# Kernel tuning notes

Measured on AMD Instinct MI355X. Metric: run time of the kernel, lower is better.

Reference implementation:

```python
import jax, jax.numpy as jnp
import numpy as np

PRED_LEN = 24
F, I, H = 64, 128, 512  # features_size, input_size, hidden_size
B, S = 1024, 168        # batch, seq_len


def setup_inputs() -> dict:
    key = jax.random.key(0)
    ks = jax.random.split(key, 14)
    s = 0.05
    return {
        "x": jax.random.normal(ks[0], (B, S, F), dtype=jnp.float32),
        "W_enc": jax.random.normal(ks[1], (I, F), dtype=jnp.float32) * s,
        "b_enc": jax.random.normal(ks[2], (I,), dtype=jnp.float32) * s,
        "Wih0": jax.random.normal(ks[3], (4 * H, I), dtype=jnp.float32) * s,
        "Whh0": jax.random.normal(ks[4], (4 * H, H), dtype=jnp.float32) * s,
        "bih0": jax.random.normal(ks[5], (4 * H,), dtype=jnp.float32) * s,
        "bhh0": jax.random.normal(ks[6], (4 * H,), dtype=jnp.float32) * s,
        "Wih1": jax.random.normal(ks[7], (4 * H, H), dtype=jnp.float32) * s,
        "Whh1": jax.random.normal(ks[8], (4 * H, H), dtype=jnp.float32) * s,
        "bih1": jax.random.normal(ks[9], (4 * H,), dtype=jnp.float32) * s,
        "bhh1": jax.random.normal(ks[10], (4 * H,), dtype=jnp.float32) * s,
        "W_dec": jax.random.normal(ks[11], (F, H), dtype=jnp.float32) * s,
        "b_dec": jax.random.normal(ks[12], (F,), dtype=jnp.float32) * s,
    }


def _lstm_cell(xt, h, c, Wih, Whh, bih, bhh):
    # PyTorch gate order: i, f, g, o
    gates = xt @ Wih.T + h @ Whh.T + (bih + bhh)
    i, f, g, o = jnp.split(gates, 4, axis=-1)
    c = jax.nn.sigmoid(f) * c + jax.nn.sigmoid(i) * jnp.tanh(g)
    h = jax.nn.sigmoid(o) * jnp.tanh(c)
    return h, c


def reference(x, W_enc, b_enc, Wih0, Whh0, bih0, bhh0,
              Wih1, Whh1, bih1, bhh1, W_dec, b_dec):
    batch = x.shape[0]
    h0 = jnp.zeros((batch, H), x.dtype)
    init = (h0, h0, h0, h0)  # (h_l0, c_l0, h_l1, c_l1)

    def step(carry, xt):
        hl0, cl0, hl1, cl1 = carry
        enc = xt @ W_enc.T + b_enc
        hl0, cl0 = _lstm_cell(enc, hl0, cl0, Wih0, Whh0, bih0, bhh0)
        hl1, cl1 = _lstm_cell(hl0, hl1, cl1, Wih1, Whh1, bih1, bhh1)
        out = hl1 @ W_dec.T + b_dec
        return (hl0, cl0, hl1, cl1), out

    # teacher-forced pass over the observed sequence; keep only last output
    carry, outs = jax.lax.scan(step, init, jnp.transpose(x, (1, 0, 2)))
    last = outs[-1]  # [B, F], prediction for step seq_len (idx = seq_len-1)

    def ar_step(state, _):
        carry, prev = state
        carry, out = step(carry, prev)
        return (carry, out), out

    _, ar_outs = jax.lax.scan(ar_step, (carry, last), None, length=PRED_LEN - 1)
    outputs = jnp.concatenate([last[None], ar_outs], axis=0)  # [pred_len, B, F]
    return jnp.transpose(outputs, (1, 0, 2))  # [B, pred_len, F]
```

## Files before the change

### kernel.cpp

```cpp
#include <hip/hip_runtime.h>

#define B_   1024
#define S_   168
#define F_   64
#define I_   128
#define H_   512
#define G4   2048
#define PRED 24

typedef unsigned short u16;
typedef unsigned int   u32;
typedef __attribute__((ext_vector_type(8))) __bf16 bf16x8;
typedef __attribute__((ext_vector_type(4))) float  f32x4;
typedef __attribute__((ext_vector_type(4))) int    i32x4;

__device__ __forceinline__ u16 f2bf(float f) {
  u32 u = __float_as_uint(f);
  u += 0x7fff + ((u >> 16) & 1);
  return (u16)(u >> 16);
}
__device__ __forceinline__ float bf2f(u16 h) {
  return __uint_as_float(((u32)h) << 16);
}
__device__ __forceinline__ float sigm(float x) {
  x = fminf(fmaxf(x, -30.f), 30.f);
  return 1.f / (1.f + __expf(-x));
}
__device__ __forceinline__ float tanh_(float x) {
  x = fminf(fmaxf(x, -15.f), 15.f);
  float e = __expf(2.f * x);
  return (e - 1.f) / (e + 1.f);
}


__global__ void k_split(const float* __restrict__ src, u16* __restrict__ hi,
                        u16* __restrict__ lo, int n) {
  for (int i = blockIdx.x * 256 + threadIdx.x; i < n; i += gridDim.x * 256) {
    float a = src[i];
    u16 h = f2bf(a);
    hi[i] = h;
    lo[i] = f2bf(a - bf2f(h));
  }
}

__global__ void k_w0c(const float* __restrict__ Wih0, const float* __restrict__ Wenc,
                      float* __restrict__ W0c) {
  int id = blockIdx.x * 256 + threadIdx.x;
  int j = id >> 6, f = id & 63;
  float s = 0.f;
  for (int i = 0; i < 128; ++i) s += Wih0[j * 128 + i] * Wenc[i * 64 + f];
  W0c[id] = s;
}

__global__ void k_w0cd(const float* __restrict__ W0c, const float* __restrict__ Wdec,
                       float* __restrict__ W0cd) {
  int id = blockIdx.x * 256 + threadIdx.x;
  int j = id >> 9, m = id & 511;
  float s = 0.f;
  for (int f = 0; f < 64; ++f) s += W0c[j * 64 + f] * Wdec[f * 512 + m];
  W0cd[id] = s;
}

__global__ void k_biases(const float* __restrict__ Wih0, const float* __restrict__ benc,
                         const float* __restrict__ bih0, const float* __restrict__ bhh0,
                         const float* __restrict__ bih1, const float* __restrict__ bhh1,
                         float* __restrict__ b0c, float* __restrict__ b1c) {
  int j = blockIdx.x * 256 + threadIdx.x;
  float s = 0.f;
  for (int i = 0; i < 128; ++i) s += Wih0[j * 128 + i] * benc[i];
  b0c[j] = s + bih0[j] + bhh0[j];
  b1c[j] = bih1[j] + bhh1[j];
}

__global__ void k_b0ar(const float* __restrict__ W0c, const float* __restrict__ bdec,
                       const float* __restrict__ b0c, float* __restrict__ b0ar) {
  int j = blockIdx.x * 256 + threadIdx.x;
  float s = 0.f;
  for (int f = 0; f < 64; ++f) s += W0c[j * 64 + f] * bdec[f];
  b0ar[j] = b0c[j] + s;
}

__global__ void k_pack(const float* __restrict__ W, int K, u16* __restrict__ dst) {
  int id = blockIdx.x * 256 + threadIdx.x;
  int lane = id & 63, fi = id >> 6;
  int NK = K >> 5;
  int kt = fi % NK, jg = fi / NK;
  int g = jg & 3, jt = jg >> 2;
  int j = jt * 16 + (lane & 15);
  int kb = kt * 32 + (lane >> 4) * 8;
  const float* src = W + (size_t)(g * 512 + j) * K + kb;
  u16 hi[8] __attribute__((aligned(16)));
  u16 lo[8] __attribute__((aligned(16)));
#pragma unroll
  for (int e = 0; e < 8; ++e) {
    float v = src[e];
    u16 h = f2bf(v);
    hi[e] = h;
    lo[e] = f2bf(v - bf2f(h));
  }
  u16* d = dst + (size_t)fi * 1024 + lane * 8;
  *(i32x4*)d = *(const i32x4*)hi;
  *(i32x4*)(d + 512) = *(const i32x4*)lo;
}


struct CellArgs {
  const u16* A1hi; const u16* A1lo; int strideA1; int K1;
  const u16* W1p;
  const u16* A2hi; const u16* A2lo;
  const u16* W2p;
  const float* bias;
  float* c;
  u16* hhi; u16* hlo;
};

struct DecArgs {
  const u16* hhi; const u16* hlo;
  const float* Wdec; const float* bdec;
  float* out;
};

__device__ __forceinline__ void cell_body(const CellArgs& P, u16* smem_,
                                          int t, int jblk, int mblk) {
  const u16* __restrict__ A1hi = P.A1hi;
  const u16* __restrict__ A1lo = P.A1lo;
  const int strideA1 = P.strideA1;
  const int K1 = P.K1;
  const u16* __restrict__ W1p = P.W1p;
  const u16* __restrict__ A2hi = P.A2hi;
  const u16* __restrict__ A2lo = P.A2lo;
  const u16* __restrict__ W2p = P.W2p;
  const float* __restrict__ bias = P.bias;
  float* __restrict__ c = P.c;
  u16* __restrict__ hhi = P.hhi;
  u16* __restrict__ hlo = P.hlo;

  const int mbase = mblk * 64;
  const int lane = t & 63, wv = t >> 6;
  const int kk = wv >> 1, jh = wv & 1;
  const int lr = lane & 15, qk = lane >> 4;
  const int jtg = jblk * 2 + jh;
  const int nc1 = (K1 == 64) ? 1 : 4;
  const int NC  = nc1 + 4;
  const int NK1 = K1 >> 5;

  f32x4 acc[4][4];
#pragma unroll
  for (int mi = 0; mi < 4; ++mi)
#pragma unroll
    for (int g = 0; g < 4; ++g) acc[mi][g] = (f32x4){0.f, 0.f, 0.f, 0.f};

  auto prm = [&](int cc, const u16*& Ah, const u16*& Al, int& st, int& kb, int& Kc,
                 const u16*& Wp, int& NK) {
    if (cc < nc1) { Ah = A1hi; Al = A1lo; st = strideA1; kb = cc * 128;
                    Kc = (K1 == 64) ? 64 : 128; Wp = W1p; NK = NK1; }
    else { int i = cc - nc1; Ah = A2hi; Al = A2lo; st = 512; kb = i * 128;
           Kc = 128; Wp = W2p; NK = 16; }
  };
  auto nsof = [&](int cc) { return (cc < nc1 && K1 == 64) ? 2 : 4; };

  auto stageLoad = [&](int cc, i32x4* rr) {
    const u16 *Ah, *Al, *Wp_; int st, kb, Kc, NK;
    prm(cc, Ah, Al, st, kb, Kc, Wp_, NK);
    const int ppr = Kc >> 3;
    const int npc = (Kc == 128) ? 4 : 2;
#pragma unroll 4
    for (int p = 0; p < npc; ++p) {
      int li   = p * 512 + t;
      int part = li >= 64 * ppr;
      int liw  = li - part * 64 * ppr;
      int rown = (ppr == 16) ? (liw >> 4) : (liw >> 3);
      int kp   = liw & (ppr - 1);
      const u16* src = (part ? Al : Ah) + (size_t)(mbase + rown) * st + kb + kp * 8;
      rr[p] = *(const i32x4*)src;
    }
  };
  auto stageWrite = [&](int cc, const i32x4* rr, int buf) {
    const int Kc  = (cc < nc1 && K1 == 64) ? 64 : 128;
    const int ppr = Kc >> 3;
    const int npc = (Kc == 128) ? 4 : 2;
    u16* sb = smem_ + buf * 16384;
#pragma unroll 4
    for (int p = 0; p < npc; ++p) {
      int li   = p * 512 + t;
      int part = li >= 64 * ppr;
      int liw  = li - part * 64 * ppr;
      int rown = (ppr == 16) ? (liw >> 4) : (liw >> 3);
      int kp   = liw & (ppr - 1);
      *(i32x4*)&sb[(((part * 64 + rown) * ppr) + (kp ^ (rown & (ppr - 1)))) * 8] = rr[p];
    }
  };
  auto loadW = [&](const u16* Wp_, int NK, int kt, i32x4* wh, i32x4* wl) {
#pragma unroll
    for (int g = 0; g < 4; ++g) {
      const u16* p = Wp_ + (size_t)((jtg * 4 + g) * NK + kt) * 1024 + lane * 8;
      wh[g] = *(const i32x4*)p;
      wl[g] = *(const i32x4*)(p + 512);
    }
  };
  auto mstep = [&](int buf, int ppr, const i32x4* wh, const i32x4* wl) {
    const u16* sb = smem_ + buf * 16384;
    bf16x8 ah[4], al[4];
#pragma unroll
    for (int mi = 0; mi < 4; ++mi) {
      int rowA = mi * 16 + lr;
      int pl   = (kk * 4 + qk) ^ (rowA & (ppr - 1));
      ah[mi] = *(const bf16x8*)&sb[(rowA * ppr + pl) * 8];
      al[mi] = *(const bf16x8*)&sb[((64 + rowA) * ppr + pl) * 8];
    }
#pragma unroll
    for (int g = 0; g < 4; ++g) {
      bf16x8 bh = __builtin_bit_cast(bf16x8, wh[g]);
      bf16x8 bl = __builtin_bit_cast(bf16x8, wl[g]);
#pragma unroll
      for (int mi = 0; mi < 4; ++mi) {
        acc[mi][g] = __builtin_amdgcn_mfma_f32_16x16x32_bf16(ah[mi], bh, acc[mi][g], 0, 0, 0);
        acc[mi][g] = __builtin_amdgcn_mfma_f32_16x16x32_bf16(al[mi], bh, acc[mi][g], 0, 0, 0);
        acc[mi][g] = __builtin_amdgcn_mfma_f32_16x16x32_bf16(ah[mi], bl, acc[mi][g], 0, 0, 0);
      }
    }
  };

  i32x4 sreg[4];
  i32x4 whA[4], wlA[4], whB[4], wlB[4];

  stageLoad(0, sreg);
  stageWrite(0, sreg, 0);
  {
    const u16 *Ah, *Al, *Wp_; int st, kb, Kc, NK;
    prm(0, Ah, Al, st, kb, Kc, Wp_, NK);
    if (kk < nsof(0)) loadW(Wp_, NK, (kb >> 5) + kk, whA, wlA);
  }
  __syncthreads();

  for (int cc = 0; cc < NC; ++cc) {
    const int buf  = cc & 1;
    const bool more = (cc + 1 < NC);
    if (more) {
      stageLoad(cc + 1, sreg);
      const u16 *Ah, *Al, *Wp_; int st, kb, Kc, NK;
      prm(cc + 1, Ah, Al, st, kb, Kc, Wp_, NK);
      if (kk < nsof(cc + 1)) loadW(Wp_, NK, (kb >> 5) + kk, whB, wlB);
    }
    {
      const u16 *Ah, *Al, *Wp_; int st, kb, Kc, NK;
      prm(cc, Ah, Al, st, kb, Kc, Wp_, NK);
      if (kk < nsof(cc)) mstep(buf, Kc >> 3, whA, wlA);
    }
    if (more) stageWrite(cc + 1, sreg, buf ^ 1);
    __syncthreads();
    if (more) {
#pragma unroll
      for (int g = 0; g < 4; ++g) { whA[g] = whB[g]; wlA[g] = wlB[g]; }
    }
  }

  float* red = (float*)smem_;
#pragma unroll
  for (int mi = 0; mi < 4; ++mi) {
    if (mi != kk) {
      int slot = kk - (kk > mi ? 1 : 0);
      float* base = red + (size_t)(((jh * 4 + mi) * 3 + slot) * 1024) + lane * 4;
#pragma unroll
      for (int g = 0; g < 4; ++g) *(f32x4*)(base + g * 256) = acc[mi][g];
    }
  }
  __syncthreads();

  f32x4 r[4];
#pragma unroll
  for (int g = 0; g < 4; ++g) r[g] = acc[0][g];
  if (kk == 1) {
#pragma unroll
    for (int g = 0; g < 4; ++g) r[g] = acc[1][g];
  } else if (kk == 2) {
#pragma unroll
    for (int g = 0; g < 4; ++g) r[g] = acc[2][g];
  } else if (kk == 3) {
#pragma unroll
    for (int g = 0; g < 4; ++g) r[g] = acc[3][g];
  }
#pragma unroll
  for (int s = 0; s < 3; ++s) {
    float* base = red + (size_t)(((jh * 4 + kk) * 3 + s) * 1024) + lane * 4;
#pragma unroll
    for (int g = 0; g < 4; ++g) r[g] += *(const f32x4*)(base + g * 256);
  }

  const int   j   = jblk * 32 + jh * 16 + lr;
  const float bi  = bias[j];
  const float bff = bias[512 + j];
  const float bg  = bias[1024 + j];
  const float bo  = bias[1536 + j];
#pragma unroll
  for (int rr = 0; rr < 4; ++rr) {
    int b   = mbase + kk * 16 + qk * 4 + rr;
    int idx = b * 512 + j;
    float iv = sigm(r[0][rr] + bi);
    float fv = sigm(r[1][rr] + bff);
    float gv = tanh_(r[2][rr] + bg);
    float ov = sigm(r[3][rr] + bo);
    float cn = fv * c[idx] + iv * gv;
    c[idx] = cn;
    float hn = ov * tanh_(cn);
    u16 hh = f2bf(hn);
    hhi[idx] = hh;
    hlo[idx] = f2bf(hn - bf2f(hh));
  }
}

__device__ __forceinline__ void dec_body(const DecArgs& D, float* smemf,
                                         int t, int bx, int by) {
  if (by >= 8) return;
  float (*sH)[65] = (float (*)[65])smemf;
  const int bbase = bx * 64;
  const int mbase = by * 64;
  {
    int b  = bbase + (t >> 3);
    int m0 = (t & 7) * 8;
    i32x4 hv = *(const i32x4*)&D.hhi[(size_t)b * 512 + mbase + m0];
    i32x4 lv = *(const i32x4*)&D.hlo[(size_t)b * 512 + mbase + m0];
    const u16* hp = (const u16*)&hv;
    const u16* lp = (const u16*)&lv;
#pragma unroll
    for (int e = 0; e < 8; ++e)
      sH[t >> 3][m0 + e] = bf2f(hp[e]) + bf2f(lp[e]);
  }
  __syncthreads();
  const int bl = t & 63;
  const int wv = t >> 6;
  float acc[8];
#pragma unroll
  for (int u = 0; u < 8; ++u) acc[u] = 0.f;
  for (int m = 0; m < 64; ++m) {
    float hv = sH[bl][m];
#pragma unroll
    for (int u = 0; u < 8; ++u)
      acc[u] += hv * D.Wdec[(size_t)(u * 8 + wv) * 512 + mbase + m];
  }
#pragma unroll
  for (int u = 0; u < 8; ++u) {
    int f = u * 8 + wv;
    float v = acc[u];
    if (by == 0) v += D.bdec[f];
    atomicAdd(&D.out[(size_t)(bbase + bl) * (PRED * F_) + f], v);
  }
}


__global__ __launch_bounds__(512, 2) void lstm3(CellArgs a) {
  __shared__ __align__(16) u16 smem_[49152];
  cell_body(a, smem_, threadIdx.x, blockIdx.x, blockIdx.y);
}

__global__ __launch_bounds__(512, 2) void lstm3_dual(CellArgs a0, CellArgs a1) {
  __shared__ __align__(16) u16 smem_[49152];
  if (blockIdx.z == 0) cell_body(a0, smem_, threadIdx.x, blockIdx.x, blockIdx.y);
  else                 cell_body(a1, smem_, threadIdx.x, blockIdx.x, blockIdx.y);
}

__global__ __launch_bounds__(512, 2) void lstm3_cell_dec(CellArgs a, DecArgs d) {
  __shared__ __align__(16) u16 smem_[49152];
  if (blockIdx.z == 0) cell_body(a, smem_, threadIdx.x, blockIdx.x, blockIdx.y);
  else                 dec_body(d, (float*)smem_, threadIdx.x, blockIdx.x, blockIdx.y);
}

__global__ __launch_bounds__(512) void k_decoder2(DecArgs d) {
  __shared__ __align__(16) float sm[64 * 65];
  dec_body(d, sm, threadIdx.x, blockIdx.x, blockIdx.y);
}


extern "C" void kernel_launch(void* const* d_in, const int* in_sizes, int n_in,
                              void* d_out, int out_size, void* d_ws, size_t ws_size,
                              hipStream_t stream) {
  const float* x    = (const float*)d_in[0];
  const float* Wenc = (const float*)d_in[1];
  const float* benc = (const float*)d_in[2];
  const float* Wih0 = (const float*)d_in[3];
  const float* Whh0 = (const float*)d_in[4];
  const float* bih0 = (const float*)d_in[5];
  const float* bhh0 = (const float*)d_in[6];
  const float* Wih1 = (const float*)d_in[7];
  const float* Whh1 = (const float*)d_in[8];
  const float* bih1 = (const float*)d_in[9];
  const float* bhh1 = (const float*)d_in[10];
  const float* Wdec = (const float*)d_in[11];
  const float* bdec = (const float*)d_in[12];
  float* out = (float*)d_out;

  char* p = (char*)d_ws;
  auto carve = [&](size_t bytes) { char* r = p; p += (bytes + 255) & ~(size_t)255; return r; };
  const size_t NX = (size_t)B_ * S_ * F_;
  const size_t NH = (size_t)B_ * H_;
  const size_t WP512 = (size_t)G4 * 512 * 2;
  u16* Xhi    = (u16*)carve(NX * 2);
  u16* Xlo    = (u16*)carve(NX * 2);
  float* W0c  = (float*)carve((size_t)G4 * 64 * 4);
  float* W0cd = (float*)carve((size_t)G4 * 512 * 4);
  u16* W0cp   = (u16*)carve((size_t)G4 * 64 * 2 * 2);
  u16* W0cdp  = (u16*)carve(WP512 * 2);
  u16* Whh0p  = (u16*)carve(WP512 * 2);
  u16* Wih1p  = (u16*)carve(WP512 * 2);
  u16* Whh1p  = (u16*)carve(WP512 * 2);
  float* b0c  = (float*)carve(G4 * 4);
  float* b0ar = (float*)carve(G4 * 4);
  float* b1c  = (float*)carve(G4 * 4);
  u16* h0hi[2] = {(u16*)carve(NH * 2), (u16*)carve(NH * 2)};
  u16* h0lo[2] = {(u16*)carve(NH * 2), (u16*)carve(NH * 2)};
  u16* h1hi[2] = {(u16*)carve(NH * 2), (u16*)carve(NH * 2)};
  u16* h1lo[2] = {(u16*)carve(NH * 2), (u16*)carve(NH * 2)};
  float* c0 = (float*)carve(NH * 4);
  float* c1 = (float*)carve(NH * 4);
  (void)ws_size; (void)n_in; (void)in_sizes;

  hipMemsetAsync(d_out, 0, (size_t)out_size * 4, stream);
  hipMemsetAsync(h0hi[0], 0, NH * 2, stream);
  hipMemsetAsync(h0lo[0], 0, NH * 2, stream);
  hipMemsetAsync(h1hi[0], 0, NH * 2, stream);
  hipMemsetAsync(h1lo[0], 0, NH * 2, stream);
  hipMemsetAsync(c0, 0, NH * 4, stream);
  hipMemsetAsync(c1, 0, NH * 4, stream);

  k_split<<<4096, 256, 0, stream>>>(x, Xhi, Xlo, (int)NX);
  k_w0c<<<512, 256, 0, stream>>>(Wih0, Wenc, W0c);
  k_w0cd<<<4096, 256, 0, stream>>>(W0c, Wdec, W0cd);
  k_biases<<<8, 256, 0, stream>>>(Wih0, benc, bih0, bhh0, bih1, bhh1, b0c, b1c);
  k_b0ar<<<8, 256, 0, stream>>>(W0c, bdec, b0c, b0ar);
  k_pack<<<32 * 16, 256, 0, stream>>>(Whh0, 512, Whh0p);
  k_pack<<<32 * 16, 256, 0, stream>>>(Wih1, 512, Wih1p);
  k_pack<<<32 * 16, 256, 0, stream>>>(Whh1, 512, Whh1p);
  k_pack<<<32 * 16, 256, 0, stream>>>(W0cd, 512, W0cdp);
  k_pack<<<32 * 2, 256, 0, stream>>>(W0c, 64, W0cp);

  dim3 grid(16, 16);
  dim3 grid2(16, 16, 2);

  {
    CellArgs l0 = {Xhi, Xlo, S_ * F_, 64, W0cp,
                   h0hi[0], h0lo[0], Whh0p, b0c, c0, h0hi[1], h0lo[1]};
    lstm3<<<grid, 512, 0, stream>>>(l0);
  }
  for (int s = 0; s < S_ - 1; ++s) {
    int pp = s & 1, np = 1 - pp;
    CellArgs l1 = {h0hi[np], h0lo[np], 512, 512, Wih1p,
                   h1hi[pp], h1lo[pp], Whh1p, b1c, c1, h1hi[np], h1lo[np]};
    CellArgs l0 = {Xhi + (size_t)(s + 1) * F_, Xlo + (size_t)(s + 1) * F_, S_ * F_, 64, W0cp,
                   h0hi[np], h0lo[np], Whh0p, b0c, c0, h0hi[pp], h0lo[pp]};
    lstm3_dual<<<grid2, 512, 0, stream>>>(l1, l0);
  }
  {
    CellArgs l1 = {h0hi[0], h0lo[0], 512, 512, Wih1p,
                   h1hi[1], h1lo[1], Whh1p, b1c, c1, h1hi[0], h1lo[0]};
    lstm3<<<grid, 512, 0, stream>>>(l1);
  }

  for (int s = S_ - 1; s < S_ + PRED - 1; ++s) {
    int pp = s & 1, np = 1 - pp;
    DecArgs d = {h1hi[np], h1lo[np], Wdec, bdec, out + (size_t)(s - (S_ - 1)) * F_};
    if (s + 1 < S_ + PRED - 1) {
      CellArgs l0 = {h1hi[np], h1lo[np], 512, 512, W0cdp,
                     h0hi[np], h0lo[np], Whh0p, b0ar, c0, h0hi[pp], h0lo[pp]};
      lstm3_cell_dec<<<grid2, 512, 0, stream>>>(l0, d);
      CellArgs l1 = {h0hi[pp], h0lo[pp], 512, 512, Wih1p,
                     h1hi[np], h1lo[np], Whh1p, b1c, c1, h1hi[pp], h1lo[pp]};
      lstm3<<<grid, 512, 0, stream>>>(l1);
    } else {
      k_decoder2<<<dim3(16, 8), 512, 0, stream>>>(d);
    }
  }
}
```

Baseline: 7.975 ms.

## Replace per-step kernel launches with a persistent cooperative kernel using grid sync

Replaces about 190 per-timestep kernel launches with one cooperative persistent kernel of 256 blocks that loops over all encoder and autoregressive steps and separates dependent phases with grid.sync(). Layer 1 and layer 0 cells now run one after the other inside each block instead of in parallel across a doubled grid, so each step uses half as many blocks. The goal is to remove launch overhead and inter-kernel gaps. The trade-off is grid-wide barrier cost and the loss of the 2x block parallelism within each step.

```diff
diff --git a/kernel.cpp b/kernel.cpp
--- a/kernel.cpp
+++ b/kernel.cpp
@@ -1,4 +1,7 @@
 #include <hip/hip_runtime.h>
+#include <hip/hip_cooperative_groups.h>
+
+namespace cg = cooperative_groups;
 
 #define B_   1024
 #define S_   168
@@ -348,26 +351,67 @@
 }
 
 
-__global__ __launch_bounds__(512, 2) void lstm3(CellArgs a) {
+struct PersistArgs {
+  const u16* Xhi; const u16* Xlo;
+  const u16 *W0cp, *W0cdp, *Whh0p, *Wih1p, *Whh1p;
+  const float *b0c, *b0ar, *b1c;
+  float *c0, *c1;
+  u16 *h0hi0, *h0hi1, *h0lo0, *h0lo1;
+  u16 *h1hi0, *h1hi1, *h1lo0, *h1lo1;
+  const float *Wdec, *bdec;
+  float* out;
+};
+
+__global__ __launch_bounds__(512, 2) void lstm_persist(PersistArgs A) {
   __shared__ __align__(16) u16 smem_[49152];
-  cell_body(a, smem_, threadIdx.x, blockIdx.x, blockIdx.y);
-}
-
-__global__ __launch_bounds__(512, 2) void lstm3_dual(CellArgs a0, CellArgs a1) {
-  __shared__ __align__(16) u16 smem_[49152];
-  if (blockIdx.z == 0) cell_body(a0, smem_, threadIdx.x, blockIdx.x, blockIdx.y);
-  else                 cell_body(a1, smem_, threadIdx.x, blockIdx.x, blockIdx.y);
-}
-
-__global__ __launch_bounds__(512, 2) void lstm3_cell_dec(CellArgs a, DecArgs d) {
-  __shared__ __align__(16) u16 smem_[49152];
-  if (blockIdx.z == 0) cell_body(a, smem_, threadIdx.x, blockIdx.x, blockIdx.y);
-  else                 dec_body(d, (float*)smem_, threadIdx.x, blockIdx.x, blockIdx.y);
-}
-
-__global__ __launch_bounds__(512) void k_decoder2(DecArgs d) {
-  __shared__ __align__(16) float sm[64 * 65];
-  dec_body(d, sm, threadIdx.x, blockIdx.x, blockIdx.y);
+  cg::grid_group grid = cg::this_grid();
+  const int t    = threadIdx.x;
+  const int bid  = blockIdx.x;
+  const int jblk = bid & 15, mblk = bid >> 4;
+
+  for (int s = -1; s <= S_ - 1; ++s) {
+    const int pp = s & 1;
+    u16* h0hiP = pp ? A.h0hi1 : A.h0hi0;  u16* h0loP = pp ? A.h0lo1 : A.h0lo0;
+    u16* h0hiN = pp ? A.h0hi0 : A.h0hi1;  u16* h0loN = pp ? A.h0lo0 : A.h0lo1;
+    u16* h1hiP = pp ? A.h1hi1 : A.h1hi0;  u16* h1loP = pp ? A.h1lo1 : A.h1lo0;
+    u16* h1hiN = pp ? A.h1hi0 : A.h1hi1;  u16* h1loN = pp ? A.h1lo0 : A.h1lo1;
+    if (s >= 0) {
+      CellArgs l1 = {h0hiN, h0loN, 512, 512, A.Wih1p,
+                     h1hiP, h1loP, A.Whh1p, A.b1c, A.c1, h1hiN, h1loN};
+      cell_body(l1, smem_, t, jblk, mblk);
+      __syncthreads();
+    }
+    if (s + 1 < S_) {
+      CellArgs l0 = {A.Xhi + (size_t)(s + 1) * F_, A.Xlo + (size_t)(s + 1) * F_,
+                     S_ * F_, 64, A.W0cp,
+                     h0hiN, h0loN, A.Whh0p, A.b0c, A.c0, h0hiP, h0loP};
+      cell_body(l0, smem_, t, jblk, mblk);
+    }
+    grid.sync();
+  }
+
+  for (int s = S_ - 1; s < S_ + PRED - 1; ++s) {
+    const int pp = s & 1;
+    u16* h0hiP = pp ? A.h0hi1 : A.h0hi0;  u16* h0loP = pp ? A.h0lo1 : A.h0lo0;
+    u16* h0hiN = pp ? A.h0hi0 : A.h0hi1;  u16* h0loN = pp ? A.h0lo0 : A.h0lo1;
+    u16* h1hiP = pp ? A.h1hi1 : A.h1hi0;  u16* h1loP = pp ? A.h1lo1 : A.h1lo0;
+    u16* h1hiN = pp ? A.h1hi0 : A.h1hi1;  u16* h1loN = pp ? A.h1lo0 : A.h1lo1;
+    DecArgs d = {h1hiN, h1loN, A.Wdec, A.bdec, A.out + (size_t)(s - (S_ - 1)) * F_};
+    if (s + 1 < S_ + PRED - 1) {
+      CellArgs l0 = {h1hiN, h1loN, 512, 512, A.W0cdp,
+                     h0hiN, h0loN, A.Whh0p, A.b0ar, A.c0, h0hiP, h0loP};
+      cell_body(l0, smem_, t, jblk, mblk);
+      __syncthreads();
+      if (bid < 128) dec_body(d, (float*)smem_, t, bid & 15, bid >> 4);
+      grid.sync();
+      CellArgs l1 = {h0hiP, h0loP, 512, 512, A.Wih1p,
+                     h1hiN, h1loN, A.Whh1p, A.b1c, A.c1, h1hiP, h1loP};
+      cell_body(l1, smem_, t, jblk, mblk);
+      grid.sync();
+    } else {
+      if (bid < 128) dec_body(d, (float*)smem_, t, bid & 15, bid >> 4);
+    }
+  }
 }
 
 
@@ -433,40 +477,19 @@
   k_pack<<<32 * 16, 256, 0, stream>>>(W0cd, 512, W0cdp);
   k_pack<<<32 * 2, 256, 0, stream>>>(W0c, 64, W0cp);
 
-  dim3 grid(16, 16);
-  dim3 grid2(16, 16, 2);
-
-  {
-    CellArgs l0 = {Xhi, Xlo, S_ * F_, 64, W0cp,
-                   h0hi[0], h0lo[0], Whh0p, b0c, c0, h0hi[1], h0lo[1]};
-    lstm3<<<grid, 512, 0, stream>>>(l0);
-  }
-  for (int s = 0; s < S_ - 1; ++s) {
-    int pp = s & 1, np = 1 - pp;
-    CellArgs l1 = {h0hi[np], h0lo[np], 512, 512, Wih1p,
-                   h1hi[pp], h1lo[pp], Whh1p, b1c, c1, h1hi[np], h1lo[np]};
-    CellArgs l0 = {Xhi + (size_t)(s + 1) * F_, Xlo + (size_t)(s + 1) * F_, S_ * F_, 64, W0cp,
-                   h0hi[np], h0lo[np], Whh0p, b0c, c0, h0hi[pp], h0lo[pp]};
-    lstm3_dual<<<grid2, 512, 0, stream>>>(l1, l0);
-  }
-  {
-    CellArgs l1 = {h0hi[0], h0lo[0], 512, 512, Wih1p,
-                   h1hi[1], h1lo[1], Whh1p, b1c, c1, h1hi[0], h1lo[0]};
-    lstm3<<<grid, 512, 0, stream>>>(l1);
-  }
-
-  for (int s = S_ - 1; s < S_ + PRED - 1; ++s) {
-    int pp = s & 1, np = 1 - pp;
-    DecArgs d = {h1hi[np], h1lo[np], Wdec, bdec, out + (size_t)(s - (S_ - 1)) * F_};
-    if (s + 1 < S_ + PRED - 1) {
-      CellArgs l0 = {h1hi[np], h1lo[np], 512, 512, W0cdp,
-                     h0hi[np], h0lo[np], Whh0p, b0ar, c0, h0hi[pp], h0lo[pp]};
-      lstm3_cell_dec<<<grid2, 512, 0, stream>>>(l0, d);
-      CellArgs l1 = {h0hi[pp], h0lo[pp], 512, 512, Wih1p,
-                     h1hi[np], h1lo[np], Whh1p, b1c, c1, h1hi[pp], h1lo[pp]};
-      lstm3<<<grid, 512, 0, stream>>>(l1);
-    } else {
-      k_decoder2<<<dim3(16, 8), 512, 0, stream>>>(d);
-    }
-  }
-}
+  PersistArgs pa;
+  pa.Xhi = Xhi; pa.Xlo = Xlo;
+  pa.W0cp = W0cp; pa.W0cdp = W0cdp; pa.Whh0p = Whh0p;
+  pa.Wih1p = Wih1p; pa.Whh1p = Whh1p;
+  pa.b0c = b0c; pa.b0ar = b0ar; pa.b1c = b1c;
+  pa.c0 = c0; pa.c1 = c1;
+  pa.h0hi0 = h0hi[0]; pa.h0hi1 = h0hi[1];
+  pa.h0lo0 = h0lo[0]; pa.h0lo1 = h0lo[1];
+  pa.h1hi0 = h1hi[0]; pa.h1hi1 = h1hi[1];
+  pa.h1lo0 = h1lo[0]; pa.h1lo1 = h1lo[1];
+  pa.Wdec = Wdec; pa.bdec = bdec; pa.out = out;
+
+  void* kargs[] = { (void*)&pa };
+  hipLaunchCooperativeKernel((const void*)lstm_persist, dim3(256), dim3(512),
+                             kargs, 0, stream);
+}
```

New measurement: 16.24 ms. 104% more time.

## Split LSTM cell GEMM across waves by M rows instead of K, drop reduction

Applied to the files above, without the earlier changes.

Each wave now owns one 16-row M slice over the full K range, where before each wave owned a K slice across all 64 rows. This removes the cross-wave LDS reduction and its extra barrier, and shrinks the accumulators from 16 to 4 vectors, so registers and shared memory drop enough for launch bounds of 4 blocks per SM instead of 2. The trade-off is that weight fragments are no longer prefetched a chunk ahead; they are loaded inside the inner k loop, and every wave now reads all the weights, which raises weight traffic per block.

```diff
diff --git a/kernel.cpp b/kernel.cpp
--- a/kernel.cpp
+++ b/kernel.cpp
@@ -137,18 +137,16 @@
 
   const int mbase = mblk * 64;
   const int lane = t & 63, wv = t >> 6;
-  const int kk = wv >> 1, jh = wv & 1;
+  const int mi = wv >> 1, jh = wv & 1;
   const int lr = lane & 15, qk = lane >> 4;
   const int jtg = jblk * 2 + jh;
   const int nc1 = (K1 == 64) ? 1 : 4;
   const int NC  = nc1 + 4;
   const int NK1 = K1 >> 5;
 
-  f32x4 acc[4][4];
-#pragma unroll
-  for (int mi = 0; mi < 4; ++mi)
-#pragma unroll
-    for (int g = 0; g < 4; ++g) acc[mi][g] = (f32x4){0.f, 0.f, 0.f, 0.f};
+  f32x4 acc[4];
+#pragma unroll
+  for (int g = 0; g < 4; ++g) acc[g] = (f32x4){0.f, 0.f, 0.f, 0.f};
 
   auto prm = [&](int cc, const u16*& Ah, const u16*& Al, int& st, int& kb, int& Kc,
                  const u16*& Wp, int& NK) {
@@ -157,7 +155,6 @@
     else { int i = cc - nc1; Ah = A2hi; Al = A2lo; st = 512; kb = i * 128;
            Kc = 128; Wp = W2p; NK = 16; }
   };
-  auto nsof = [&](int cc) { return (cc < nc1 && K1 == 64) ? 2 : 4; };
 
   auto stageLoad = [&](int cc, i32x4* rr) {
     const u16 *Ah, *Al, *Wp_; int st, kb, Kc, NK;
@@ -198,93 +195,46 @@
       wl[g] = *(const i32x4*)(p + 512);
     }
   };
-  auto mstep = [&](int buf, int ppr, const i32x4* wh, const i32x4* wl) {
+  auto mstep = [&](int buf, int ppr, const u16* Wp_, int NK, int kb5) {
     const u16* sb = smem_ + buf * 16384;
-    bf16x8 ah[4], al[4];
-#pragma unroll
-    for (int mi = 0; mi < 4; ++mi) {
-      int rowA = mi * 16 + lr;
-      int pl   = (kk * 4 + qk) ^ (rowA & (ppr - 1));
-      ah[mi] = *(const bf16x8*)&sb[(rowA * ppr + pl) * 8];
-      al[mi] = *(const bf16x8*)&sb[((64 + rowA) * ppr + pl) * 8];
-    }
-#pragma unroll
-    for (int g = 0; g < 4; ++g) {
-      bf16x8 bh = __builtin_bit_cast(bf16x8, wh[g]);
-      bf16x8 bl = __builtin_bit_cast(bf16x8, wl[g]);
-#pragma unroll
-      for (int mi = 0; mi < 4; ++mi) {
-        acc[mi][g] = __builtin_amdgcn_mfma_f32_16x16x32_bf16(ah[mi], bh, acc[mi][g], 0, 0, 0);
-        acc[mi][g] = __builtin_amdgcn_mfma_f32_16x16x32_bf16(al[mi], bh, acc[mi][g], 0, 0, 0);
-        acc[mi][g] = __builtin_amdgcn_mfma_f32_16x16x32_bf16(ah[mi], bl, acc[mi][g], 0, 0, 0);
+    const int nkt  = ppr >> 2;
+    const int rowA = mi * 16 + lr;
+    const int rmask = rowA & (ppr - 1);
+#pragma unroll 4
+    for (int kt = 0; kt < nkt; ++kt) {
+      i32x4 wh[4], wl[4];
+      loadW(Wp_, NK, kb5 + kt, wh, wl);
+      int pl = (kt * 4 + qk) ^ rmask;
+      bf16x8 ah = *(const bf16x8*)&sb[(rowA * ppr + pl) * 8];
+      bf16x8 al = *(const bf16x8*)&sb[((64 + rowA) * ppr + pl) * 8];
+#pragma unroll
+      for (int g = 0; g < 4; ++g) {
+        bf16x8 bh = __builtin_bit_cast(bf16x8, wh[g]);
+        bf16x8 bl = __builtin_bit_cast(bf16x8, wl[g]);
+        acc[g] = __builtin_amdgcn_mfma_f32_16x16x32_bf16(ah, bh, acc[g], 0, 0, 0);
+        acc[g] = __builtin_amdgcn_mfma_f32_16x16x32_bf16(al, bh, acc[g], 0, 0, 0);
+        acc[g] = __builtin_amdgcn_mfma_f32_16x16x32_bf16(ah, bl, acc[g], 0, 0, 0);
       }
     }
   };
 
   i32x4 sreg[4];
-  i32x4 whA[4], wlA[4], whB[4], wlB[4];
 
   stageLoad(0, sreg);
   stageWrite(0, sreg, 0);
-  {
-    const u16 *Ah, *Al, *Wp_; int st, kb, Kc, NK;
-    prm(0, Ah, Al, st, kb, Kc, Wp_, NK);
-    if (kk < nsof(0)) loadW(Wp_, NK, (kb >> 5) + kk, whA, wlA);
-  }
   __syncthreads();
 
   for (int cc = 0; cc < NC; ++cc) {
     const int buf  = cc & 1;
     const bool more = (cc + 1 < NC);
-    if (more) {
-      stageLoad(cc + 1, sreg);
-      const u16 *Ah, *Al, *Wp_; int st, kb, Kc, NK;
-      prm(cc + 1, Ah, Al, st, kb, Kc, Wp_, NK);
-      if (kk < nsof(cc + 1)) loadW(Wp_, NK, (kb >> 5) + kk, whB, wlB);
-    }
+    if (more) stageLoad(cc + 1, sreg);
     {
       const u16 *Ah, *Al, *Wp_; int st, kb, Kc, NK;
       prm(cc, Ah, Al, st, kb, Kc, Wp_, NK);
-      if (kk < nsof(cc)) mstep(buf, Kc >> 3, whA, wlA);
+      mstep(buf, Kc >> 3, Wp_, NK, kb >> 5);
     }
     if (more) stageWrite(cc + 1, sreg, buf ^ 1);
     __syncthreads();
-    if (more) {
-#pragma unroll
-      for (int g = 0; g < 4; ++g) { whA[g] = whB[g]; wlA[g] = wlB[g]; }
-    }
-  }
-
-  float* red = (float*)smem_;
-#pragma unroll
-  for (int mi = 0; mi < 4; ++mi) {
-    if (mi != kk) {
-      int slot = kk - (kk > mi ? 1 : 0);
-      float* base = red + (size_t)(((jh * 4 + mi) * 3 + slot) * 1024) + lane * 4;
-#pragma unroll
-      for (int g = 0; g < 4; ++g) *(f32x4*)(base + g * 256) = acc[mi][g];
-    }
-  }
-  __syncthreads();
-
-  f32x4 r[4];
-#pragma unroll
-  for (int g = 0; g < 4; ++g) r[g] = acc[0][g];
-  if (kk == 1) {
-#pragma unroll
-    for (int g = 0; g < 4; ++g) r[g] = acc[1][g];
-  } else if (kk == 2) {
-#pragma unroll
-    for (int g = 0; g < 4; ++g) r[g] = acc[2][g];
-  } else if (kk == 3) {
-#pragma unroll
-    for (int g = 0; g < 4; ++g) r[g] = acc[3][g];
-  }
-#pragma unroll
-  for (int s = 0; s < 3; ++s) {
-    float* base = red + (size_t)(((jh * 4 + kk) * 3 + s) * 1024) + lane * 4;
-#pragma unroll
-    for (int g = 0; g < 4; ++g) r[g] += *(const f32x4*)(base + g * 256);
   }
 
   const int   j   = jblk * 32 + jh * 16 + lr;
@@ -294,12 +244,12 @@
   const float bo  = bias[1536 + j];
 #pragma unroll
   for (int rr = 0; rr < 4; ++rr) {
-    int b   = mbase + kk * 16 + qk * 4 + rr;
+    int b   = mbase + mi * 16 + qk * 4 + rr;
     int idx = b * 512 + j;
-    float iv = sigm(r[0][rr] + bi);
-    float fv = sigm(r[1][rr] + bff);
-    float gv = tanh_(r[2][rr] + bg);
-    float ov = sigm(r[3][rr] + bo);
+    float iv = sigm(acc[0][rr] + bi);
+    float fv = sigm(acc[1][rr] + bff);
+    float gv = tanh_(acc[2][rr] + bg);
+    float ov = sigm(acc[3][rr] + bo);
     float cn = fv * c[idx] + iv * gv;
     c[idx] = cn;
     float hn = ov * tanh_(cn);
@@ -348,19 +298,19 @@
 }
 
 
-__global__ __launch_bounds__(512, 2) void lstm3(CellArgs a) {
-  __shared__ __align__(16) u16 smem_[49152];
+__global__ __launch_bounds__(512, 4) void lstm3(CellArgs a) {
+  __shared__ __align__(16) u16 smem_[32768];
   cell_body(a, smem_, threadIdx.x, blockIdx.x, blockIdx.y);
 }
 
-__global__ __launch_bounds__(512, 2) void lstm3_dual(CellArgs a0, CellArgs a1) {
-  __shared__ __align__(16) u16 smem_[49152];
+__global__ __launch_bounds__(512, 4) void lstm3_dual(CellArgs a0, CellArgs a1) {
+  __shared__ __align__(16) u16 smem_[32768];
   if (blockIdx.z == 0) cell_body(a0, smem_, threadIdx.x, blockIdx.x, blockIdx.y);
   else                 cell_body(a1, smem_, threadIdx.x, blockIdx.x, blockIdx.y);
 }
 
-__global__ __launch_bounds__(512, 2) void lstm3_cell_dec(CellArgs a, DecArgs d) {
-  __shared__ __align__(16) u16 smem_[49152];
+__global__ __launch_bounds__(512, 4) void lstm3_cell_dec(CellArgs a, DecArgs d) {
+  __shared__ __align__(16) u16 smem_[32768];
   if (blockIdx.z == 0) cell_body(a, smem_, threadIdx.x, blockIdx.x, blockIdx.y);
   else                 dec_body(d, (float*)smem_, threadIdx.x, blockIdx.x, blockIdx.y);
 }
```

Measured after the change: 8.297 ms. 1.04x slower.
